# Performance work log

Measured on AMD Instinct MI355X. Metric: run time of the kernel, lower is better.

Reference implementation:

```python
import jax, jax.numpy as jnp
import numpy as np

B, S, D, H = 2, 2048, 1024, 16
DK = D // H


def setup_inputs() -> dict:
    key = jax.random.key(0)
    ks = jax.random.split(key, 12)
    scale = 0.02  # keep exp(QK^T) finite in fp32
    return {
        "query": jax.random.normal(ks[0], (B, S, D), jnp.float32),
        "key_": jax.random.normal(ks[1], (B, S, D), jnp.float32),
        "value": jax.random.normal(ks[2], (B, S, D), jnp.float32),
        "mask": jax.random.randint(ks[3], (B, S, S), 0, 2, jnp.int32),
        "Wq": scale * jax.random.normal(ks[4], (D, D), jnp.float32),
        "bq": jnp.zeros((D,), jnp.float32),
        "Wk": scale * jax.random.normal(ks[5], (D, D), jnp.float32),
        "bk": jnp.zeros((D,), jnp.float32),
        "Wv": scale * jax.random.normal(ks[6], (D, D), jnp.float32),
        "bv": jnp.zeros((D,), jnp.float32),
        "Wo": scale * jax.random.normal(ks[7], (D, D), jnp.float32),
        "bo": jnp.zeros((D,), jnp.float32),
    }


def reference(query, key_, value, mask, Wq, bq, Wk, bk, Wv, bv, Wo, bo):
    b, s, d = query.shape
    # torch Linear: x @ W.T + b, then split heads -> [b, h, s, d_k]
    def proj(x, W, bias):
        return (x @ W.T + bias).reshape(b, s, H, DK).transpose(0, 2, 1, 3)

    q = proj(query, Wq, bq)
    k = proj(key_, Wk, bk)
    v = proj(value, Wv, bv)

    # non-standard: exp(QK^T) / sqrt(d_k), then mask, then softmax
    scores = jnp.exp(jnp.einsum("bhqd,bhkd->bhqk", q, k)) / jnp.sqrt(
        jnp.asarray(DK, q.dtype)
    )
    scores = jnp.where(mask[:, None, :, :] == 0, jnp.asarray(-1e9, q.dtype), scores)
    p_attn = jax.nn.softmax(scores, axis=-1)

    out = jnp.einsum("bhqk,bhkd->bhqd", p_attn, v)  # [b, h, s, d_k]
    out = out.transpose(0, 2, 1, 3).reshape(b, s, d)  # merge heads
    return out @ Wo.T + bo
```

## Files before the change

### kernel.cpp

```cpp
#include <hip/hip_runtime.h>
#include <math.h>

#define B_ 2
#define S_ 2048
#define D_ 1024
#define H_ 16
#define DK_ 64
#define M_ (B_*S_)

typedef __attribute__((ext_vector_type(8))) _Float16 f16x8;
typedef __attribute__((ext_vector_type(4))) _Float16 f16x4;
typedef __attribute__((ext_vector_type(2))) __fp16 fp16x2;
typedef __attribute__((ext_vector_type(4))) float f32x4;

#define MFMA16(a,b,c) __builtin_amdgcn_mfma_f32_16x16x32_f16((a),(b),(c),0,0,0)

__device__ __forceinline__ void gload16(const void* g, void* l) {
    __builtin_amdgcn_global_load_lds(
        (const __attribute__((address_space(1))) unsigned int*)g,
        (__attribute__((address_space(3))) unsigned int*)l, 16, 0, 0);
}

__global__ __launch_bounds__(256)
void splitall(const float* __restrict__ query, const float* __restrict__ key_,
              const float* __restrict__ value,
              const float* __restrict__ Wq, const float* __restrict__ Wk,
              const float* __restrict__ Wv, const float* __restrict__ Wo,
              _Float16* __restrict__ Xhq, _Float16* __restrict__ Xlq,
              _Float16* __restrict__ Xhk, _Float16* __restrict__ Xlk,
              _Float16* __restrict__ Xhv,
              _Float16* __restrict__ hq, _Float16* __restrict__ lq,
              _Float16* __restrict__ hk, _Float16* __restrict__ lk,
              _Float16* __restrict__ hv, _Float16* __restrict__ ho)
{
    int t = blockIdx.x * 256 + threadIdx.x;
    int region = t >> 19;
    int u = t & 524287;
    const float* src; _Float16* dhi; _Float16* dlo; size_t e;
    if (region < 3) {
        e = (size_t)u * 8;
        src = (region == 0) ? query : (region == 1) ? key_ : value;
        dhi = (region == 0) ? Xhq : (region == 1) ? Xhk : Xhv;
        dlo = (region == 0) ? Xlq : (region == 1) ? Xlk : nullptr;
    } else {
        int mi = u >> 17;
        e = (size_t)(u & 131071) * 8;
        src = (mi == 0) ? Wq : (mi == 1) ? Wk : (mi == 2) ? Wv : Wo;
        dhi = (mi == 0) ? hq : (mi == 1) ? hk : (mi == 2) ? hv : ho;
        dlo = (mi == 0) ? lq : (mi == 1) ? lk : nullptr;
    }
    float4 a = *(const float4*)&src[e];
    float4 b = *(const float4*)&src[e + 4];
    float v[8] = {a.x, a.y, a.z, a.w, b.x, b.y, b.z, b.w};
    f16x8 hi, lo;
    #pragma unroll
    for (int j = 0; j < 8; ++j) {
        float s = v[j] * 64.f;
        _Float16 h = (_Float16)s;
        hi[j] = h; lo[j] = (_Float16)(s - (float)h);
    }
    *(f16x8*)&dhi[e] = hi;
    if (dlo) *(f16x8*)&dlo[e] = lo;
}

__global__ __launch_bounds__(256)
void maskpack(const int* __restrict__ mask, unsigned long long* __restrict__ mbits)
{
    int wid  = (blockIdx.x * 256 + threadIdx.x) >> 6;
    int lane = threadIdx.x & 63;
    int v = mask[(size_t)wid * 64 + lane];
    unsigned long long bal = __ballot(v != 0);
    if (lane == 0) mbits[wid] = bal;
}

template<int NPROD, int OUT_MODE>
__device__ __forceinline__
void gemm_body2(char* smem, const _Float16* __restrict__ Ah,
                const _Float16* __restrict__ Al,
                const _Float16* __restrict__ Bh, const _Float16* __restrict__ Bl,
                const float* __restrict__ bias, void* __restrict__ outp, int gid)
{
    constexpr int BUFSZ = (NPROD == 3) ? 32768 : 16384;
    const int tid  = threadIdx.x;
    const int lane = tid & 63, w = tid >> 6;
    const int lx   = lane & 15, lg = lane >> 4;
    const int wm   = w >> 1, wn = w & 1;

    int nid = (gid & 7) * 32 + (gid >> 3);
    const int colBase = (nid & 7) * 128;
    const int rowBase = (nid >> 3) * 128;

    const int sRow = (lane >> 2);
    const int sChk = (lane & 3) ^ ((lane >> 2) & 3);

    auto STAGE = [&](int buf, int k0) {
        char* base = smem + buf * BUFSZ;
        #pragma unroll
        for (int ii = 0; ii < 2; ++ii) {
            int i = w * 2 + ii;
            int r = i * 16 + sRow;
            gload16(Ah + (size_t)(rowBase + r) * D_ + k0 + sChk * 8, base + i * 1024);
            gload16(Bh + (size_t)(colBase + r) * D_ + k0 + sChk * 8, base + 8192 + i * 1024);
            if (NPROD == 3) {
                gload16(Al + (size_t)(rowBase + r) * D_ + k0 + sChk * 8, base + 16384 + i * 1024);
                gload16(Bl + (size_t)(colBase + r) * D_ + k0 + sChk * 8, base + 24576 + i * 1024);
            }
        }
    };

    f32x4 acc[4][4];
    #pragma unroll
    for (int i = 0; i < 4; ++i)
        #pragma unroll
        for (int j = 0; j < 4; ++j) acc[i][j] = (f32x4){0.f, 0.f, 0.f, 0.f};

    STAGE(0, 0);
    __syncthreads();
    int cur = 0;
    for (int k0 = 0; k0 < D_; k0 += 32) {
        if (k0 + 32 < D_) STAGE(cur ^ 1, k0 + 32);
        char* base = smem + cur * BUFSZ;
        _Float16* AhS = (_Float16*)base;
        _Float16* BhS = (_Float16*)(base + 8192);
        _Float16* AlS = (_Float16*)(base + 16384);
        _Float16* BlS = (_Float16*)(base + 24576);

        f16x8 bh[4], bl[4];
        #pragma unroll
        for (int fj = 0; fj < 4; ++fj) {
            int brow = wn * 64 + fj * 16 + lx;
            bh[fj] = *(const f16x8*)((char*)BhS + brow * 64 + 16 * (lg ^ (brow & 3)));
            if (NPROD == 3)
                bl[fj] = *(const f16x8*)((char*)BlS + brow * 64 + 16 * (lg ^ (brow & 3)));
        }
        #pragma unroll
        for (int fi = 0; fi < 4; ++fi) {
            int arow = wm * 64 + fi * 16 + lx;
            f16x8 ah = *(const f16x8*)((char*)AhS + arow * 64 + 16 * (lg ^ (arow & 3)));
            f16x8 al;
            if (NPROD == 3)
                al = *(const f16x8*)((char*)AlS + arow * 64 + 16 * (lg ^ (arow & 3)));
            #pragma unroll
            for (int fj = 0; fj < 4; ++fj) {
                acc[fi][fj] = MFMA16(ah, bh[fj], acc[fi][fj]);
                if (NPROD == 3) {
                    acc[fi][fj] = MFMA16(ah, bl[fj], acc[fi][fj]);
                    acc[fi][fj] = MFMA16(al, bh[fj], acc[fi][fj]);
                }
            }
        }
        __syncthreads();
        cur ^= 1;
    }

    constexpr float INV = 1.f / 4096.f;
    #pragma unroll
    for (int fi = 0; fi < 4; ++fi) {
        #pragma unroll
        for (int fj = 0; fj < 4; ++fj) {
            int n = colBase + wn * 64 + fj * 16 + lx;
            float bv = bias[n];
            if (OUT_MODE == 1) {
                _Float16* Ohi = (_Float16*)outp;
                _Float16* Olo = Ohi + (size_t)M_ * D_;
                int hh = n >> 6, d = n & 63;
                #pragma unroll
                for (int rr = 0; rr < 4; ++rr) {
                    int m = rowBase + wm * 64 + fi * 16 + lg * 4 + rr;
                    int bb = m >> 11, s = m & 2047;
                    float val = acc[fi][fj][rr] * INV + bv;
                    _Float16 hv = (_Float16)val;
                    size_t o = (((size_t)bb * H_ + hh) * S_ + s) * DK_ + d;
                    Ohi[o] = hv;
                    Olo[o] = (_Float16)(val - (float)hv);
                }
            } else {
                _Float16* Vt = (_Float16*)outp;
                int hh = n >> 6, d = n & 63;
                int m0 = rowBase + wm * 64 + fi * 16 + lg * 4;
                int bb = m0 >> 11, s = m0 & 2047;
                f16x4 pk;
                #pragma unroll
                for (int rr = 0; rr < 4; ++rr)
                    pk[rr] = (_Float16)(acc[fi][fj][rr] * INV + bv);
                *(f16x4*)&Vt[(((size_t)bb * H_ + hh) * DK_ + d) * S_ + s] = pk;
            }
        }
    }
}

__global__ __launch_bounds__(256)
void proj3(const _Float16* __restrict__ Xhq, const _Float16* __restrict__ Xlq,
           const _Float16* __restrict__ Xhk, const _Float16* __restrict__ Xlk,
           const _Float16* __restrict__ Xhv,
           const _Float16* __restrict__ WhiQ, const _Float16* __restrict__ WloQ,
           const _Float16* __restrict__ WhiK, const _Float16* __restrict__ WloK,
           const _Float16* __restrict__ WhiV,
           const float* __restrict__ bq, const float* __restrict__ bk,
           const float* __restrict__ bv,
           _Float16* __restrict__ Qhi, _Float16* __restrict__ Khi,
           _Float16* __restrict__ VtW)
{
    extern __shared__ char smem[];
    int mode = blockIdx.x >> 8;
    int gid  = blockIdx.x & 255;
    if (mode == 0)
        gemm_body2<3, 1>(smem, Xhq, Xlq, WhiQ, WloQ, bq, Qhi, gid);
    else if (mode == 1)
        gemm_body2<3, 1>(smem, Xhk, Xlk, WhiK, WloK, bk, Khi, gid);
    else
        gemm_body2<1, 2>(smem, Xhv, nullptr, WhiV, nullptr, bv, VtW, gid);
}

__global__ __launch_bounds__(256)
void gemm64(const _Float16* __restrict__ Ap, const _Float16* __restrict__ Bhi,
            const float* __restrict__ bias, float* __restrict__ out)
{
    __shared__ __attribute__((aligned(16))) char smem[24576];

    const int tid  = threadIdx.x;
    const int lane = tid & 63, w = tid >> 6;
    const int lx   = lane & 15, lg = lane >> 4;
    const int wm   = w >> 1, wn = w & 1;

    int gid = blockIdx.x;
    int nid = (gid & 7) * 64 + (gid >> 3);
    const int colBase = (nid & 7) * 128;
    const int rowBase = (nid >> 3) * 64;

    const int sRow = (lane >> 2);
    const int sChk = (lane & 3) ^ ((lane >> 2) & 3);

    auto STAGE = [&](int buf, int k0) {
        char* base = smem + buf * 12288;
        gload16(Ap + (size_t)(rowBase + w * 16 + sRow) * D_ + k0 + sChk * 8,
                base + w * 1024);
        #pragma unroll
        for (int ii = 0; ii < 2; ++ii) {
            int i = w * 2 + ii;
            int r = i * 16 + sRow;
            gload16(Bhi + (size_t)(colBase + r) * D_ + k0 + sChk * 8,
                    base + 4096 + i * 1024);
        }
    };

    f32x4 acc[2][4];
    #pragma unroll
    for (int i = 0; i < 2; ++i)
        #pragma unroll
        for (int j = 0; j < 4; ++j) acc[i][j] = (f32x4){0.f, 0.f, 0.f, 0.f};

    STAGE(0, 0);
    __syncthreads();
    int cur = 0;
    for (int k0 = 0; k0 < D_; k0 += 32) {
        if (k0 + 32 < D_) STAGE(cur ^ 1, k0 + 32);
        char* base = smem + cur * 12288;
        _Float16* AS = (_Float16*)base;
        _Float16* BS = (_Float16*)(base + 4096);

        f16x8 bh[4];
        #pragma unroll
        for (int fj = 0; fj < 4; ++fj) {
            int brow = wn * 64 + fj * 16 + lx;
            bh[fj] = *(const f16x8*)((char*)BS + brow * 64 + 16 * (lg ^ (brow & 3)));
        }
        #pragma unroll
        for (int fi = 0; fi < 2; ++fi) {
            int arow = wm * 32 + fi * 16 + lx;
            f16x8 ah = *(const f16x8*)((char*)AS + arow * 64 + 16 * (lg ^ (arow & 3)));
            #pragma unroll
            for (int fj = 0; fj < 4; ++fj)
                acc[fi][fj] = MFMA16(ah, bh[fj], acc[fi][fj]);
        }
        __syncthreads();
        cur ^= 1;
    }

    constexpr float INV = 1.f / 64.f;
    #pragma unroll
    for (int fi = 0; fi < 2; ++fi) {
        #pragma unroll
        for (int fj = 0; fj < 4; ++fj) {
            int n = colBase + wn * 64 + fj * 16 + lx;
            float bv = bias[n];
            #pragma unroll
            for (int rr = 0; rr < 4; ++rr) {
                int m = rowBase + wm * 32 + fi * 16 + lg * 4 + rr;
                out[(size_t)m * D_ + n] = acc[fi][fj][rr] * INV + bv;
            }
        }
    }
}

__global__ __launch_bounds__(512, 4)
void flash_mfma(const _Float16* __restrict__ Qhi, const _Float16* __restrict__ Qlo,
                const _Float16* __restrict__ Khi, const _Float16* __restrict__ Klo,
                const _Float16* __restrict__ Vt, const unsigned long long* __restrict__ Mb,
                _Float16* __restrict__ octx)
{
    __shared__ __attribute__((aligned(16))) _Float16 KhiS[64 * 64];
    __shared__ __attribute__((aligned(16))) _Float16 KloS[64 * 64];
    __shared__ __attribute__((aligned(16))) _Float16 VtS[64 * 64];
    __shared__ __attribute__((aligned(16))) _Float16 PwS[8][16 * 64];

    const int tid  = threadIdx.x;
    const int lane = tid & 63;
    const int w    = tid >> 6;
    const int lx   = lane & 15;
    const int lg   = lane >> 4;

    int bid = blockIdx.x;
    int swz = (bid & 7) * 64 + (bid >> 3);
    int qb = swz & 15;
    int h  = (swz >> 4) & 15;
    int b  = swz >> 8;

    const int q0 = qb * 128;
    const size_t bh = (size_t)b * H_ + h;
    const _Float16* KhiG = Khi + bh * S_ * DK_;
    const _Float16* KloG = Klo + bh * S_ * DK_;
    const _Float16* VtG  = Vt  + bh * DK_ * S_;

    const int qrow = q0 + w * 16 + lx;
    f16x8 qh[2], ql[2];
    {
        const _Float16* ph = Qhi + bh * S_ * DK_ + (size_t)qrow * DK_ + lg * 8;
        const _Float16* pl = Qlo + bh * S_ * DK_ + (size_t)qrow * DK_ + lg * 8;
        qh[0] = *(const f16x8*)ph;
        qh[1] = *(const f16x8*)(ph + 32);
        ql[0] = *(const f16x8*)pl;
        ql[1] = *(const f16x8*)(pl + 32);
    }

    f32x4 oacc[4];
    float m_run = -1e30f, l_run = 0.f;
    #pragma unroll
    for (int dt = 0; dt < 4; ++dt) oacc[dt] = (f32x4){0.f, 0.f, 0.f, 0.f};

    char* Pw = (char*)&PwS[w][0];
    const unsigned long long* mrow = Mb + ((size_t)b * S_ + qrow) * (S_ / 64);

    for (int s0 = 0; s0 < S_; s0 += 64) {
        __syncthreads();

        {
            int rr = w * 8 + (lane >> 3);
            int cc = (lane & 7) ^ (lane >> 3);
            gload16(KhiG + (size_t)(s0 + rr) * DK_ + cc * 8, &KhiS[w * 512]);
            gload16(KloG + (size_t)(s0 + rr) * DK_ + cc * 8, &KloS[w * 512]);
            gload16(VtG + (size_t)rr * S_ + s0 + cc * 8, &VtS[w * 512]);
        }
        unsigned long long mw = mrow[s0 >> 6];
        __syncthreads();

        float sv[4][4];
        #pragma unroll
        for (int ct = 0; ct < 4; ++ct) {
            int row  = ct * 16 + lx;
            int sw   = (row & 7) << 4;
            int base = row * 128 + lg * 16;
            f16x8 kh0 = *(const f16x8*)((const char*)KhiS + ((base +  0) ^ sw));
            f16x8 kh1 = *(const f16x8*)((const char*)KhiS + ((base + 64) ^ sw));
            f16x8 kl0 = *(const f16x8*)((const char*)KloS + ((base +  0) ^ sw));
            f16x8 kl1 = *(const f16x8*)((const char*)KloS + ((base + 64) ^ sw));
            f32x4 s = (f32x4){0.f, 0.f, 0.f, 0.f};
            s = MFMA16(kh0, qh[0], s);
            s = MFMA16(kh1, qh[1], s);
            s = MFMA16(kl0, qh[0], s);
            s = MFMA16(kl1, qh[1], s);
            s = MFMA16(kh0, ql[0], s);
            s = MFMA16(kh1, ql[1], s);
            #pragma unroll
            for (int r = 0; r < 4; ++r) sv[ct][r] = s[r];
        }

        unsigned long long ms = mw >> (lg * 4);
        float tv[16];
        #pragma unroll
        for (int ct = 0; ct < 4; ++ct)
            #pragma unroll
            for (int r = 0; r < 4; ++r) {
                float e = __expf(sv[ct][r] - 2.0794415416798357f);
                tv[ct * 4 + r] = ((ms >> (ct * 16 + r)) & 1ull) ? e : -1e30f;
            }
        float m01 = fmaxf(fmaxf(tv[0], tv[1]), fmaxf(tv[2], tv[3]));
        float m23 = fmaxf(fmaxf(tv[4], tv[5]), fmaxf(tv[6], tv[7]));
        float m45 = fmaxf(fmaxf(tv[8], tv[9]), fmaxf(tv[10], tv[11]));
        float m67 = fmaxf(fmaxf(tv[12], tv[13]), fmaxf(tv[14], tv[15]));
        float tmax = fmaxf(fmaxf(m01, m23), fmaxf(m45, m67));
        tmax = fmaxf(tmax, __shfl_xor(tmax, 16));
        tmax = fmaxf(tmax, __shfl_xor(tmax, 32));

        if (__any(tmax > m_run)) {
            float mn = fmaxf(m_run, tmax);
            float scl = __expf(m_run - mn);
            m_run = mn;
            l_run *= scl;
            #pragma unroll
            for (int dt = 0; dt < 4; ++dt)
                #pragma unroll
                for (int r = 0; r < 4; ++r) oacc[dt][r] *= scl;
        }
        float mr = m_run;
        float pp[16], sum = 0.f;
        #pragma unroll
        for (int i = 0; i < 16; ++i) {
            pp[i] = __expf(tv[i] - mr);
            sum += pp[i];
        }
        sum += __shfl_xor(sum, 16);
        sum += __shfl_xor(sum, 32);
        l_run += sum;

        {
            int psw = (lx & 7) << 4;
            #pragma unroll
            for (int ct = 0; ct < 4; ++ct) {
                fp16x2 a = __builtin_amdgcn_cvt_pkrtz(pp[ct * 4 + 0], pp[ct * 4 + 1]);
                fp16x2 c = __builtin_amdgcn_cvt_pkrtz(pp[ct * 4 + 2], pp[ct * 4 + 3]);
                unsigned int au, cu;
                __builtin_memcpy(&au, &a, 4);
                __builtin_memcpy(&cu, &c, 4);
                int off = lx * 128 + ct * 32 + lg * 8;
                *(unsigned int*)(Pw + ((off + 0) ^ psw)) = au;
                *(unsigned int*)(Pw + ((off + 4) ^ psw)) = cu;
            }
        }

        f16x8 pa0, pa1;
        {
            int psw = (lx & 7) << 4;
            int pb  = lx * 128 + lg * 16;
            pa0 = *(const f16x8*)(Pw + ((pb +  0) ^ psw));
            pa1 = *(const f16x8*)(Pw + ((pb + 64) ^ psw));
        }
        #pragma unroll
        for (int dt = 0; dt < 4; ++dt) {
            int vrow = dt * 16 + lx;
            int vs   = (vrow & 7) << 4;
            int vb   = vrow * 128 + lg * 16;
            f16x8 v0 = *(const f16x8*)((const char*)VtS + ((vb +  0) ^ vs));
            f16x8 v1 = *(const f16x8*)((const char*)VtS + ((vb + 64) ^ vs));
            oacc[dt] = MFMA16(v0, pa0, oacc[dt]);
            oacc[dt] = MFMA16(v1, pa1, oacc[dt]);
        }
    }

    {
        float inv = 1.0f / l_run;
        #pragma unroll
        for (int dt = 0; dt < 4; ++dt) {
            f16x4 o;
            #pragma unroll
            for (int r = 0; r < 4; ++r) o[r] = (_Float16)(oacc[dt][r] * inv);
            *(f16x4*)&octx[((size_t)b * S_ + qrow) * D_ + h * DK_ + dt * 16 + lg * 4] = o;
        }
    }
}

extern "C" void kernel_launch(void* const* d_in, const int* in_sizes, int n_in,
                              void* d_out, int out_size, void* d_ws, size_t ws_size,
                              hipStream_t stream)
{
    const float* query = (const float*)d_in[0];
    const float* key_  = (const float*)d_in[1];
    const float* value = (const float*)d_in[2];
    const int*   mask  = (const int*)d_in[3];
    const float* Wq = (const float*)d_in[4];
    const float* bq = (const float*)d_in[5];
    const float* Wk = (const float*)d_in[6];
    const float* bk = (const float*)d_in[7];
    const float* Wv = (const float*)d_in[8];
    const float* bv = (const float*)d_in[9];
    const float* Wo = (const float*)d_in[10];
    const float* bo = (const float*)d_in[11];

    char* p = (char*)d_ws;
    unsigned long long* mbits = (unsigned long long*)p;  p += (size_t)1 << 20;
    _Float16* WhiQ = (_Float16*)p;  p += (size_t)2 << 20;
    _Float16* WloQ = (_Float16*)p;  p += (size_t)2 << 20;
    _Float16* WhiK = (_Float16*)p;  p += (size_t)2 << 20;
    _Float16* WloK = (_Float16*)p;  p += (size_t)2 << 20;
    _Float16* WhiV = (_Float16*)p;  p += (size_t)2 << 20;
    _Float16* WhiO = (_Float16*)p;  p += (size_t)2 << 20;
    _Float16* Xhq  = (_Float16*)p;  p += (size_t)8 << 20;
    _Float16* Xlq  = (_Float16*)p;  p += (size_t)8 << 20;
    _Float16* Xhk  = (_Float16*)p;  p += (size_t)8 << 20;
    _Float16* Xlk  = (_Float16*)p;  p += (size_t)8 << 20;
    _Float16* Xhv  = (_Float16*)p;  p += (size_t)8 << 20;
    _Float16* Qhi  = (_Float16*)p;  p += (size_t)16 << 20;
    _Float16* Khi  = (_Float16*)p;  p += (size_t)16 << 20;
    _Float16* VtW  = (_Float16*)p;  p += (size_t)8 << 20;
    _Float16* octx = (_Float16*)p;  p += (size_t)8 << 20;
    float* out = (float*)d_out;

    _Float16* Qlo = Qhi + (size_t)M_ * D_;
    _Float16* Klo = Khi + (size_t)M_ * D_;

    maskpack<<<(B_ * S_ * (S_ / 64) * 64) / 256, 256, 0, stream>>>(mask, mbits);
    splitall<<<8192, 256, 0, stream>>>(query, key_, value, Wq, Wk, Wv, Wo,
                                       Xhq, Xlq, Xhk, Xlk, Xhv,
                                       WhiQ, WloQ, WhiK, WloK, WhiV, WhiO);

    proj3<<<768, 256, 65536, stream>>>(Xhq, Xlq, Xhk, Xlk, Xhv,
                                       WhiQ, WloQ, WhiK, WloK, WhiV,
                                       bq, bk, bv, Qhi, Khi, VtW);

    flash_mfma<<<512, 512, 0, stream>>>(Qhi, Qlo, Khi, Klo, VtW, mbits, octx);

    gemm64<<<512, 256, 0, stream>>>(octx, WhiO, bo, out);
}
```

Before: 211.0 us.

## Two-pass attention: compute row maxima first, skip key tiles that underflow

Splits the flash attention kernel into two passes. The first pass streams double-buffered K tiles through shared memory and records the masked per-tile, per-row score maxima. From the global row maximum it derives a threshold below which exp(exp(s)/8 - max) underflows in fp32. The second pass recomputes QK^T only for tiles that can contribute, reading K and V straight from global memory, with a fixed max so no online rescaling is needed. This saves softmax and PV work on negligible tiles, at the cost of computing QK twice for the kept tiles and using uncached global loads.

```diff
diff --git a/kernel.cpp b/kernel.cpp
--- a/kernel.cpp
+++ b/kernel.cpp
@@ -299,10 +299,8 @@
                 const _Float16* __restrict__ Vt, const unsigned long long* __restrict__ Mb,
                 _Float16* __restrict__ octx)
 {
-    __shared__ __attribute__((aligned(16))) _Float16 KhiS[64 * 64];
-    __shared__ __attribute__((aligned(16))) _Float16 KloS[64 * 64];
-    __shared__ __attribute__((aligned(16))) _Float16 VtS[64 * 64];
-    __shared__ __attribute__((aligned(16))) _Float16 PwS[8][16 * 64];
+    __shared__ __attribute__((aligned(16))) _Float16 Kbuf[2][2][64 * 64];
+    __shared__ float tmS[8][32][16];
 
     const int tid  = threadIdx.x;
     const int lane = tid & 63;
@@ -333,37 +331,35 @@
         ql[1] = *(const f16x8*)(pl + 32);
     }
 
-    f32x4 oacc[4];
-    float m_run = -1e30f, l_run = 0.f;
-    #pragma unroll
-    for (int dt = 0; dt < 4; ++dt) oacc[dt] = (f32x4){0.f, 0.f, 0.f, 0.f};
-
-    char* Pw = (char*)&PwS[w][0];
     const unsigned long long* mrow = Mb + ((size_t)b * S_ + qrow) * (S_ / 64);
-
-    for (int s0 = 0; s0 < S_; s0 += 64) {
-        __syncthreads();
-
-        {
-            int rr = w * 8 + (lane >> 3);
-            int cc = (lane & 7) ^ (lane >> 3);
-            gload16(KhiG + (size_t)(s0 + rr) * DK_ + cc * 8, &KhiS[w * 512]);
-            gload16(KloG + (size_t)(s0 + rr) * DK_ + cc * 8, &KloS[w * 512]);
-            gload16(VtG + (size_t)rr * S_ + s0 + cc * 8, &VtS[w * 512]);
-        }
-        unsigned long long mw = mrow[s0 >> 6];
-        __syncthreads();
-
-        float sv[4][4];
+    constexpr float LN8 = 2.0794415416798357f;
+
+    auto STAGEK = [&](int buf, int t) {
+        int rr = t * 64 + w * 8 + (lane >> 3);
+        int cc = (lane & 7) ^ (lane >> 3);
+        gload16(KhiG + (size_t)rr * DK_ + cc * 8, &Kbuf[buf][0][w * 512]);
+        gload16(KloG + (size_t)rr * DK_ + cc * 8, &Kbuf[buf][1][w * 512]);
+    };
+
+    float m_row = -3.0e38f;
+    STAGEK(0, 0);
+    __syncthreads();
+    int cur = 0;
+    for (int t = 0; t < 32; ++t) {
+        if (t < 31) STAGEK(cur ^ 1, t + 1);
+        unsigned long long mw = mrow[t];
+        const char* KH = (const char*)&Kbuf[cur][0][0];
+        const char* KL = (const char*)&Kbuf[cur][1][0];
+        float mx = -3.0e38f;
         #pragma unroll
         for (int ct = 0; ct < 4; ++ct) {
             int row  = ct * 16 + lx;
             int sw   = (row & 7) << 4;
             int base = row * 128 + lg * 16;
-            f16x8 kh0 = *(const f16x8*)((const char*)KhiS + ((base +  0) ^ sw));
-            f16x8 kh1 = *(const f16x8*)((const char*)KhiS + ((base + 64) ^ sw));
-            f16x8 kl0 = *(const f16x8*)((const char*)KloS + ((base +  0) ^ sw));
-            f16x8 kl1 = *(const f16x8*)((const char*)KloS + ((base + 64) ^ sw));
+            f16x8 kh0 = *(const f16x8*)(KH + ((base +  0) ^ sw));
+            f16x8 kh1 = *(const f16x8*)(KH + ((base + 64) ^ sw));
+            f16x8 kl0 = *(const f16x8*)(KL + ((base +  0) ^ sw));
+            f16x8 kl1 = *(const f16x8*)(KL + ((base + 64) ^ sw));
             f32x4 s = (f32x4){0.f, 0.f, 0.f, 0.f};
             s = MFMA16(kh0, qh[0], s);
             s = MFMA16(kh1, qh[1], s);
@@ -372,47 +368,57 @@
             s = MFMA16(kh0, ql[0], s);
             s = MFMA16(kh1, ql[1], s);
             #pragma unroll
-            for (int r = 0; r < 4; ++r) sv[ct][r] = s[r];
-        }
-
-        unsigned long long ms = mw >> (lg * 4);
-        float tv[16];
-        #pragma unroll
-        for (int ct = 0; ct < 4; ++ct)
-            #pragma unroll
             for (int r = 0; r < 4; ++r) {
-                float e = __expf(sv[ct][r] - 2.0794415416798357f);
-                tv[ct * 4 + r] = ((ms >> (ct * 16 + r)) & 1ull) ? e : -1e30f;
-            }
-        float m01 = fmaxf(fmaxf(tv[0], tv[1]), fmaxf(tv[2], tv[3]));
-        float m23 = fmaxf(fmaxf(tv[4], tv[5]), fmaxf(tv[6], tv[7]));
-        float m45 = fmaxf(fmaxf(tv[8], tv[9]), fmaxf(tv[10], tv[11]));
-        float m67 = fmaxf(fmaxf(tv[12], tv[13]), fmaxf(tv[14], tv[15]));
-        float tmax = fmaxf(fmaxf(m01, m23), fmaxf(m45, m67));
-        tmax = fmaxf(tmax, __shfl_xor(tmax, 16));
-        tmax = fmaxf(tmax, __shfl_xor(tmax, 32));
-
-        if (__any(tmax > m_run)) {
-            float mn = fmaxf(m_run, tmax);
-            float scl = __expf(m_run - mn);
-            m_run = mn;
-            l_run *= scl;
-            #pragma unroll
-            for (int dt = 0; dt < 4; ++dt)
-                #pragma unroll
-                for (int r = 0; r < 4; ++r) oacc[dt][r] *= scl;
-        }
-        float mr = m_run;
-        float pp[16], sum = 0.f;
-        #pragma unroll
-        for (int i = 0; i < 16; ++i) {
-            pp[i] = __expf(tv[i] - mr);
-            sum += pp[i];
-        }
-        sum += __shfl_xor(sum, 16);
-        sum += __shfl_xor(sum, 32);
-        l_run += sum;
-
+                float se = ((mw >> (lg * 4 + ct * 16 + r)) & 1ull) ? s[r] : -3.0e38f;
+                mx = fmaxf(mx, se);
+            }
+        }
+        mx = fmaxf(mx, __shfl_xor(mx, 16));
+        mx = fmaxf(mx, __shfl_xor(mx, 32));
+        if (lg == 0) tmS[w][t][lx] = mx;
+        m_row = fmaxf(m_row, mx);
+        __syncthreads();
+        cur ^= 1;
+    }
+
+    float tmax = __expf(m_row - LN8);
+    float thr  = (tmax > 128.f) ? m_row + logf(1.f - 87.f / tmax) : -3.0e38f;
+    __syncthreads();
+
+    char* Pw = (char*)&Kbuf[0][0][0] + w * 2048;
+    f32x4 oacc[4];
+    #pragma unroll
+    for (int dt = 0; dt < 4; ++dt) oacc[dt] = (f32x4){0.f, 0.f, 0.f, 0.f};
+    float l_lane = 0.f;
+
+    for (int t = 0; t < 32; ++t) {
+        if (__all(tmS[w][t][lx] < thr)) continue;
+        unsigned long long mw = mrow[t];
+        float pp[16];
+        #pragma unroll
+        for (int ct = 0; ct < 4; ++ct) {
+            const _Float16* kp = KhiG + (size_t)(t * 64 + ct * 16 + lx) * DK_ + lg * 8;
+            const _Float16* lp = KloG + (size_t)(t * 64 + ct * 16 + lx) * DK_ + lg * 8;
+            f16x8 kh0 = *(const f16x8*)kp;
+            f16x8 kh1 = *(const f16x8*)(kp + 32);
+            f16x8 kl0 = *(const f16x8*)lp;
+            f16x8 kl1 = *(const f16x8*)(lp + 32);
+            f32x4 s = (f32x4){0.f, 0.f, 0.f, 0.f};
+            s = MFMA16(kh0, qh[0], s);
+            s = MFMA16(kh1, qh[1], s);
+            s = MFMA16(kl0, qh[0], s);
+            s = MFMA16(kl1, qh[1], s);
+            s = MFMA16(kh0, ql[0], s);
+            s = MFMA16(kh1, ql[1], s);
+            #pragma unroll
+            for (int r = 0; r < 4; ++r) {
+                float ti = __expf(s[r] - LN8);
+                float e  = __expf(ti - tmax);
+                e = ((mw >> (lg * 4 + ct * 16 + r)) & 1ull) ? e : 0.f;
+                pp[ct * 4 + r] = e;
+                l_lane += e;
+            }
+        }
         {
             int psw = (lx & 7) << 4;
             #pragma unroll
@@ -427,7 +433,6 @@
                 *(unsigned int*)(Pw + ((off + 4) ^ psw)) = cu;
             }
         }
-
         f16x8 pa0, pa1;
         {
             int psw = (lx & 7) << 4;
@@ -437,18 +442,19 @@
         }
         #pragma unroll
         for (int dt = 0; dt < 4; ++dt) {
-            int vrow = dt * 16 + lx;
-            int vs   = (vrow & 7) << 4;
-            int vb   = vrow * 128 + lg * 16;
-            f16x8 v0 = *(const f16x8*)((const char*)VtS + ((vb +  0) ^ vs));
-            f16x8 v1 = *(const f16x8*)((const char*)VtS + ((vb + 64) ^ vs));
+            const _Float16* vp = VtG + (size_t)(dt * 16 + lx) * S_ + t * 64 + lg * 8;
+            f16x8 v0 = *(const f16x8*)vp;
+            f16x8 v1 = *(const f16x8*)(vp + 32);
             oacc[dt] = MFMA16(v0, pa0, oacc[dt]);
             oacc[dt] = MFMA16(v1, pa1, oacc[dt]);
         }
     }
 
+    float l = l_lane;
+    l += __shfl_xor(l, 16);
+    l += __shfl_xor(l, 32);
     {
-        float inv = 1.0f / l_run;
+        float inv = 1.0f / l;
         #pragma unroll
         for (int dt = 0; dt < 4; ++dt) {
             f16x4 o;
```

After: 359.8 us. 70.6% more time.
